# Kernel optimization log

Hardware: AMD Instinct MI355X
Metric: run time of the kernel (lower is better)

Reference implementation:

```python
import jax, jax.numpy as jnp
import numpy as np

# ---- config (mirrors AAModel init kwargs: ns=48, nv=10, sh_lmax=1) ----
N, E, NS, NV = 100000, 60000, 48, 10
SED, DED = 32, 32          # sigma / distance embedding dims
CUTOFF = 30.0              # GaussianSmearing(0, cutoff, DED)
SQ3 = float(np.sqrt(3.0))
W1_NUMEL = NS * NS + NS * NV                                   # 2784
# layer-2 fully-connected TP path weight offsets:
#   0e(x)0e->0e, 0e(x)1o->1o, 1o(x)0e->1o, 1o(x)1o->0e, 1o(x)1o->1e
O2 = [2304, 2784, 2884, 3364, 3464]


def _mlp2(x, W1, b1, W2, b2):
    return jax.nn.relu(x @ W1 + b1) @ W2 + b2


def _seg_mean(x, idx, n):
    s = jax.ops.segment_sum(x, idx, num_segments=n)
    cnt = jax.ops.segment_sum(jnp.ones(idx.shape, x.dtype), idx, num_segments=n)
    return s / jnp.maximum(cnt, 1.0).reshape((n,) + (1,) * (x.ndim - 1))


def _forward(pos, node_sigma_emb, node_s, edge_W1, edge_b1, edge_W2, edge_b2,
             fc1_W1, fc1_b1, fc1_W2, fc1_b2, fc2_W1, fc2_b1, fc2_W2, fc2_b2,
             edge_index):
    src, dst = edge_index[0], edge_index[1]
    vec = pos[dst] - pos[src]                          # [E,3]
    d = jnp.linalg.norm(vec, axis=-1)                  # [E]
    sh1 = SQ3 * vec / (d[:, None] + 1e-8)              # l=1 SH, component norm; sh0 == 1
    # Gaussian smearing of edge distances
    offsets = jnp.linspace(0.0, CUTOFF, DED)
    coeff = -0.5 / (offsets[1] - offsets[0]) ** 2
    demb = jnp.exp(coeff * (d[:, None] - offsets) ** 2)          # [E,DED]
    edge_emb = _mlp2(jnp.concatenate([node_sigma_emb[src], demb], -1),
                     edge_W1, edge_b1, edge_W2, edge_b2)         # [E,NS]

    # ---- conv layer 1:  ns x0e  (x)  1x0e+1x1o  ->  ns x0e + nv x1o ----
    xs = node_s[src]
    ea = jnp.concatenate([edge_emb, node_s[src], node_s[dst]], -1)   # [E,3*NS]
    w = _mlp2(ea, fc1_W1, fc1_b1, fc1_W2, fc1_b2)                    # [E,2784]
    w00 = w[:, :NS * NS].reshape(-1, NS, NS)
    w01 = w[:, NS * NS:].reshape(-1, NS, NV)
    inv = 1.0 / np.sqrt(NS)
    m_s = jnp.einsum('eio,ei->eo', w00, xs) * inv                    # [E,NS]
    m_v = jnp.einsum('eio,ei->eo', w01, xs)[:, :, None] * sh1[:, None, :] * inv  # [E,NV,3]
    node_s1 = node_s + _seg_mean(m_s, dst, N)                        # residual
    node_v1 = _seg_mean(m_v, dst, N)

    # ---- conv layer 2:  ns x0e + nv x1o  (x)  1x0e+1x1o  ->  ns x0e + nv x1o + nv x1e ----
    ea2 = jnp.concatenate([edge_emb, node_s1[src], node_s1[dst]], -1)
    w2 = _mlp2(ea2, fc2_W1, fc2_b1, fc2_W2, fc2_b2)                  # [E,3464]
    w00 = w2[:, :O2[0]].reshape(-1, NS, NS)
    w01 = w2[:, O2[0]:O2[1]].reshape(-1, NS, NV)
    w10 = w2[:, O2[1]:O2[2]].reshape(-1, NV, NV)
    w11s = w2[:, O2[2]:O2[3]].reshape(-1, NV, NS)
    w11p = w2[:, O2[3]:O2[4]].reshape(-1, NV, NV)
    xs, xv = node_s1[src], node_v1[src]
    nA = 1.0 / np.sqrt(2 * NS)
    nB = 1.0 / np.sqrt(2 * NV)
    m_s = (jnp.einsum('eio,ei->eo', w00, xs) * nA
           + jnp.einsum('eio,eid,ed->eo', w11s, xv, sh1) * (nB / SQ3))
    m_v = (jnp.einsum('eio,ei->eo', w01, xs)[:, :, None] * sh1[:, None, :] * nA
           + jnp.einsum('eio,eid->eod', w10, xv) * nB)
    m_p = jnp.einsum('eio,eid->eod', w11p, jnp.cross(xv, sh1[:, None, :])) * (1.0 / np.sqrt(2.0 * NV))
    node_s2 = node_s1 + _seg_mean(m_s, dst, N)
    node_v2 = node_v1 + _seg_mean(m_v, dst, N)
    node_p = _seg_mean(m_p, dst, N)
    # final node irreps ns x0e + nv x1o + nv x1e, flattened -> [N, 108]
    return jnp.concatenate([node_s2, node_v2.reshape(N, -1), node_p.reshape(N, -1)], -1)


def setup_inputs() -> dict:
    key = jax.random.key(0)
    k = jax.random.split(key, 10)
    f32 = jnp.float32
    def lin(kk, fi, fo):
        return jax.random.normal(kk, (fi, fo), f32) / np.sqrt(fi)
    return {
        'pos': 10.0 * jax.random.normal(k[0], (N, 3), f32),
        'node_sigma_emb': jax.random.normal(k[1], (N, SED), f32),
        'node_s': jax.random.normal(k[2], (N, NS), f32),
        'edge_W1': lin(k[3], SED + DED, NS), 'edge_b1': jnp.zeros((NS,), f32),
        'edge_W2': lin(k[4], NS, NS), 'edge_b2': jnp.zeros((NS,), f32),
        'fc1_W1': lin(k[5], 3 * NS, 3 * NS), 'fc1_b1': jnp.zeros((3 * NS,), f32),
        'fc1_W2': lin(k[6], 3 * NS, W1_NUMEL), 'fc1_b2': jnp.zeros((W1_NUMEL,), f32),
        'fc2_W1': lin(k[7], 3 * NS, 3 * NS), 'fc2_b1': jnp.zeros((3 * NS,), f32),
        'fc2_W2': lin(k[8], 3 * NS, O2[-1]), 'fc2_b2': jnp.zeros((O2[-1],), f32),
        'edge_index': jax.random.randint(k[9], (2, E), 0, N, jnp.int32),
    }


def reference(pos, node_sigma_emb, node_s, edge_W1, edge_b1, edge_W2, edge_b2,
              fc1_W1, fc1_b1, fc1_W2, fc1_b2, fc2_W1, fc2_b1, fc2_W2, fc2_b2,
              edge_index):
    return _forward(pos, node_sigma_emb, node_s, edge_W1, edge_b1, edge_W2, edge_b2,
                    fc1_W1, fc1_b1, fc1_W2, fc1_b2, fc2_W1, fc2_b1, fc2_W2, fc2_b2,
                    edge_index)
```

## Files before the change

kernel.cpp:

```cpp
#include <hip/hip_runtime.h>
#include <math.h>


constexpr float SQ3f = 1.7320508075688772f;
constexpr float INV1 = 0.14433756729740643f;
constexpr float NAc  = 0.10206207261596575f;
constexpr float NBc  = 0.22360679774997896f;
constexpr float C20  = 0.22360679774997896f;
constexpr float RATIO= 1.2649110640673518f;
constexpr float DSP  = 30.0f/31.0f;
constexpr float GCOEF= -0.5f/(DSP*DSP);

typedef __attribute__((ext_vector_type(8))) short bf16x8;
typedef __attribute__((ext_vector_type(4))) float f32x4;

__device__ __forceinline__ unsigned short f2bf(float x) {
    unsigned u = __builtin_bit_cast(unsigned, x);
    u += 0x7fffu + ((u >> 16) & 1u);
    return (unsigned short)(u >> 16);
}

__device__ __forceinline__ int colmap(int layer, int t, int lm) {
    if (layer == 0) return t*16 + lm;
    if (layer == 1) {
        if (t < 144) { const int og=t/48, i=t-og*48; return i*48 + og*16 + lm; }
        const int i = t-144; return (lm<10) ? 2304 + i*10 + lm : -1;
    }
    if (t < 144) { const int og=t/48, i=t-og*48; return i*48 + og*16 + lm; }
    if (t < 174) { const int s=t-144, og=s/10, i=s-og*10; return 2884 + i*48 + og*16 + lm; }
    if (t < 222) { const int i=t-174; return (lm<10) ? 2304 + i*10 + lm : -1; }
    if (t < 232) { const int i=t-222; return (lm<10) ? 2784 + i*10 + lm : -1; }
    { const int i=t-232; return (lm<10) ? 3364 + i*10 + lm : -1; }
}

__global__ __launch_bounds__(256)
void cvt_swz(const float* __restrict__ W, const float* __restrict__ bias,
             short* __restrict__ Wsw, int ncol, int ntile, int layer)
{
    const int gid = blockIdx.x*256 + threadIdx.x;
    const int g = gid >> 6, lane = gid & 63;
    if (g >= ntile*5) return;
    const int tile = g/5, ks = g - tile*5;
    const int c  = colmap(layer, tile, lane & 15);
    const int k0 = ks*32 + (lane >> 4)*8;
    union { uint4 u4; unsigned short h[8]; } pk;
    #pragma unroll
    for (int j=0;j<8;j++) {
        const int k = k0 + j;
        float v = 0.f;
        if (c >= 0) {
            if (k < 144)       v = W[(size_t)k*ncol + c];
            else if (k == 144) v = bias[c];
        }
        pk.h[j] = f2bf(v);
    }
    *(uint4*)&Wsw[((size_t)g*64 + lane)*8] = pk.u4;
}

__global__ __launch_bounds__(256)
void edge_kernel(const float* __restrict__ pos, const float* __restrict__ sigma,
                 const int* __restrict__ ei,
                 const float* __restrict__ W1, const float* __restrict__ b1,
                 const float* __restrict__ W2, const float* __restrict__ b2,
                 float* __restrict__ edge_emb, float* __restrict__ sh1buf,
                 int* __restrict__ deg, int E)
{
    __shared__ float inl[4][64];
    __shared__ float hidl[4][48];
    const int w    = threadIdx.x >> 6;
    const int lane = threadIdx.x & 63;
    const int e    = blockIdx.x*4 + w;
    const bool valid = (e < E);
    const int ec = valid ? e : 0;
    const int src = ei[ec], dst = ei[E+ec];
    const float vx = pos[dst*3+0]-pos[src*3+0];
    const float vy = pos[dst*3+1]-pos[src*3+1];
    const float vz = pos[dst*3+2]-pos[src*3+2];
    const float d  = sqrtf(vx*vx+vy*vy+vz*vz);
    const float si = SQ3f/(d+1e-8f);
    const float s0 = vx*si, s1 = vy*si, s2 = vz*si;
    if (lane < 32) {
        inl[w][lane] = sigma[src*32+lane];
    } else {
        const float off  = (float)(lane-32)*DSP;
        const float diff = d - off;
        inl[w][lane] = expf(GCOEF*diff*diff);
    }
    __syncthreads();
    if (lane < 48) {
        float a = b1[lane];
        #pragma unroll 8
        for (int j=0;j<64;j++) a = fmaf(inl[w][j], W1[j*48+lane], a);
        hidl[w][lane] = fmaxf(a, 0.f);
    }
    __syncthreads();
    if (valid) {
        if (lane < 48) {
            float a = b2[lane];
            #pragma unroll 8
            for (int j=0;j<48;j++) a = fmaf(hidl[w][j], W2[j*48+lane], a);
            edge_emb[e*48+lane] = a;
        }
        if (lane == 0) atomicAdd(&deg[dst], 1);
        if (lane < 3)  sh1buf[e*4+lane] = (lane==0)?s0:((lane==1)?s1:s2);
    }
}

__device__ __forceinline__ void load_bfrag(const short* __restrict__ Wsw,
                                           int tile, int lane, bf16x8 (&b)[5]) {
    #pragma unroll
    for (int ks=0; ks<5; ks++)
        b[ks] = *(const bf16x8*)&Wsw[((size_t)(tile*5+ks)*64 + lane)*8];
}

__device__ __forceinline__ void mfma5(const bf16x8 (&ag)[2][5], const bf16x8 (&b)[5],
                                      f32x4& a0, f32x4& a1) {
    a0 = (f32x4){0.f,0.f,0.f,0.f};
    a1 = (f32x4){0.f,0.f,0.f,0.f};
    #pragma unroll
    for (int ks=0; ks<5; ks++) {
        a0 = __builtin_amdgcn_mfma_f32_16x16x32_bf16(ag[0][ks], b[ks], a0, 0,0,0);
        a1 = __builtin_amdgcn_mfma_f32_16x16x32_bf16(ag[1][ks], b[ks], a1, 0,0,0);
    }
}

template<typename F>
__device__ __forceinline__ void region1(const short* __restrict__ Wsw, int base,
                                        int count, int lane,
                                        const bf16x8 (&ag)[2][5], F&& upd)
{
    bf16x8 bc[5], bn[5];
    load_bfrag(Wsw, base, lane, bc);
    for (int i=0; i<count; ++i) {
        if (i+1 < count) load_bfrag(Wsw, base+i+1, lane, bn);
        f32x4 a0, a1;
        mfma5(ag, bc, a0, a1);
        upd(i, a0, a1);
        #pragma unroll
        for (int ks=0; ks<5; ks++) bc[ks] = bn[ks];
    }
}

template<int LAYER>
__global__ __launch_bounds__(256)
void conv_kernel(const float* __restrict__ edge_emb, const float* __restrict__ sh1buf,
                 const int* __restrict__ ei,
                 const float* __restrict__ sin_, const float* __restrict__ vin,
                 const short* __restrict__ W1sw, const short* __restrict__ W2sw,
                 float* __restrict__ outS, float* __restrict__ outV, int E)
{
    __shared__ __align__(16) short eaB[32*192];
    __shared__ __align__(16) short hidB[32*192];
    __shared__ __align__(16) float xsT[48][36];
    __shared__ float sh1l[32][4];
    __shared__ int   srcl[32], dstl[32];
    __shared__ __align__(16) float xvT[LAYER==2 ? 30 : 1][36];
    __shared__ __align__(16) float uT [LAYER==2 ? 10 : 1][36];
    __shared__ __align__(16) float cvT[LAYER==2 ? 30 : 1][36];

    const int t  = threadIdx.x;
    const int eb = blockIdx.x * 32;

    if (t < 32) {
        const int ge = eb + t; const int gc = (ge < E) ? ge : (E-1);
        srcl[t] = ei[gc]; dstl[t] = ei[E+gc];
    }
    if (t < 128) {
        const int e = t >> 2, k = t & 3;
        const int ge = eb + e; const int gc = (ge<E)?ge:(E-1);
        sh1l[e][k] = sh1buf[gc*4 + k];
    }
    __syncthreads();

    for (int p = t; p < 32*24; p += 256) {
        const int m = p / 24, s = p - m*24;
        const int k0 = s*8;
        float vals[8] = {0.f,0.f,0.f,0.f,0.f,0.f,0.f,0.f};
        if (k0 < 48) {
            const int ge = eb + m; const int gc = (ge<E)?ge:(E-1);
            const float4 a = *(const float4*)&edge_emb[gc*48 + k0];
            const float4 b = *(const float4*)&edge_emb[gc*48 + k0 + 4];
            vals[0]=a.x; vals[1]=a.y; vals[2]=a.z; vals[3]=a.w;
            vals[4]=b.x; vals[5]=b.y; vals[6]=b.z; vals[7]=b.w;
        } else if (k0 < 96) {
            const float4 a = *(const float4*)&sin_[srcl[m]*48 + (k0-48)];
            const float4 b = *(const float4*)&sin_[srcl[m]*48 + (k0-48) + 4];
            vals[0]=a.x; vals[1]=a.y; vals[2]=a.z; vals[3]=a.w;
            vals[4]=b.x; vals[5]=b.y; vals[6]=b.z; vals[7]=b.w;
            #pragma unroll
            for (int j=0;j<8;j++) xsT[k0-48+j][m] = vals[j];
        } else if (k0 < 144) {
            const float4 a = *(const float4*)&sin_[dstl[m]*48 + (k0-96)];
            const float4 b = *(const float4*)&sin_[dstl[m]*48 + (k0-96) + 4];
            vals[0]=a.x; vals[1]=a.y; vals[2]=a.z; vals[3]=a.w;
            vals[4]=b.x; vals[5]=b.y; vals[6]=b.z; vals[7]=b.w;
        } else if (k0 == 144) {
            vals[0] = 1.f;
        }
        union { uint4 u4; unsigned short h[8]; } pk;
        #pragma unroll
        for (int j=0;j<8;j++) pk.h[j] = f2bf(vals[j]);
        *(uint4*)&eaB[m*192 + ((s ^ (m&7))*8)] = pk.u4;
    }
    if (t < 64) {
        const int m = t >> 1, s = 18 + (t & 1);
        union { uint4 u4; unsigned short h[8]; } pk;
        pk.u4.x = pk.u4.y = pk.u4.z = pk.u4.w = 0u;
        if (s == 18) pk.h[0] = f2bf(1.f);
        *(uint4*)&hidB[m*192 + ((s ^ (m&7))*8)] = pk.u4;
    }
    if (LAYER==2) {
        for (int p=t; p<320; p+=256) {
            const int i = p >> 5, e = p & 31;
            const float x0 = vin[srcl[e]*30 + i*3+0];
            const float x1 = vin[srcl[e]*30 + i*3+1];
            const float x2 = vin[srcl[e]*30 + i*3+2];
            const float h0=sh1l[e][0], h1=sh1l[e][1], h2=sh1l[e][2];
            xvT[i*3+0][e]=x0; xvT[i*3+1][e]=x1; xvT[i*3+2][e]=x2;
            uT[i][e] = x0*h0 + x1*h1 + x2*h2;
            cvT[i*3+0][e] = x1*h2 - x2*h1;
            cvT[i*3+1][e] = x2*h0 - x0*h2;
            cvT[i*3+2][e] = x0*h1 - x1*h0;
        }
    }
    __syncthreads();

    const int wv = t >> 6, lane = t & 63;
    const int lm = lane & 15, lk = lane >> 4, lk4 = lk*4;

    {
        bf16x8 af[2][5];
        #pragma unroll
        for (int mt=0; mt<2; mt++) {
            const int m = mt*16 + lm;
            #pragma unroll
            for (int ks=0; ks<5; ks++)
                af[mt][ks] = *(const bf16x8*)&eaB[m*192 + (((ks*4+lk) ^ (m&7))*8)];
        }
        for (int nt = wv; nt < 9; nt += 4) {
            bf16x8 bw[5];
            load_bfrag(W1sw, nt, lane, bw);
            f32x4 a0, a1;
            mfma5(af, bw, a0, a1);
            const int c = nt*16 + lm;
            #pragma unroll
            for (int r=0; r<4; r++) {
                const int m0 = lk4 + r, m1 = 16 + lk4 + r;
                hidB[m0*192 + (((c>>3) ^ (m0&7))*8) + (c&7)] = (short)f2bf(fmaxf(a0[r], 0.f));
                hidB[m1*192 + (((c>>3) ^ (m1&7))*8) + (c&7)] = (short)f2bf(fmaxf(a1[r], 0.f));
            }
        }
    }
    __syncthreads();

    bf16x8 ag[2][5];
    #pragma unroll
    for (int mt=0; mt<2; mt++) {
        const int m = mt*16 + lm;
        #pragma unroll
        for (int ks=0; ks<5; ks++)
            ag[mt][ks] = *(const bf16x8*)&hidB[m*192 + (((ks*4+lk) ^ (m&7))*8)];
    }

    if (wv < 3) {
        float ms[2][4] = {{0.f,0.f,0.f,0.f},{0.f,0.f,0.f,0.f}};
        region1(W2sw, wv*48, 48, lane, ag, [&](int i, f32x4 a0, f32x4 a1) {
            const f32x4 x0 = *(const f32x4*)&xsT[i][lk4];
            const f32x4 x1 = *(const f32x4*)&xsT[i][16+lk4];
            #pragma unroll
            for (int r=0;r<4;r++) {
                ms[0][r] = fmaf(a0[r], x0[r], ms[0][r]);
                ms[1][r] = fmaf(a1[r], x1[r], ms[1][r]);
            }
        });
        if (LAYER==2) {
            region1(W2sw, 144 + wv*10, 10, lane, ag, [&](int i, f32x4 a0, f32x4 a1) {
                const f32x4 u0 = *(const f32x4*)&uT[i][lk4];
                const f32x4 u1 = *(const f32x4*)&uT[i][16+lk4];
                #pragma unroll
                for (int r=0;r<4;r++) {
                    ms[0][r] = fmaf(a0[r]*RATIO, u0[r], ms[0][r]);
                    ms[1][r] = fmaf(a1[r]*RATIO, u1[r], ms[1][r]);
                }
            });
        }
        const float scale = (LAYER==1) ? INV1 : NAc;
        const int   strd  = (LAYER==1) ? 48 : 108;
        const int o = wv*16 + lm;
        #pragma unroll
        for (int r=0;r<4;r++) {
            const int e0 = lk4+r, e1 = 16+lk4+r;
            if (eb+e0 < E) unsafeAtomicAdd(&outS[(size_t)dstl[e0]*strd + o], ms[0][r]*scale);
            if (eb+e1 < E) unsafeAtomicAdd(&outS[(size_t)dstl[e1]*strd + o], ms[1][r]*scale);
        }
    } else {
        float vc[2][4] = {{0.f,0.f,0.f,0.f},{0.f,0.f,0.f,0.f}};
        region1(W2sw, (LAYER==1) ? 144 : 174, 48, lane, ag, [&](int i, f32x4 a0, f32x4 a1) {
            const f32x4 x0 = *(const f32x4*)&xsT[i][lk4];
            const f32x4 x1 = *(const f32x4*)&xsT[i][16+lk4];
            #pragma unroll
            for (int r=0;r<4;r++) {
                vc[0][r] = fmaf(a0[r], x0[r], vc[0][r]);
                vc[1][r] = fmaf(a1[r], x1[r], vc[1][r]);
            }
        });
        if (LAYER==1) {
            if (lm < 10) {
                #pragma unroll
                for (int r=0;r<4;r++) {
                    const int e0 = lk4+r, e1 = 16+lk4+r;
                    const float v0 = vc[0][r]*INV1, v1 = vc[1][r]*INV1;
                    #pragma unroll
                    for (int d=0; d<3; d++) {
                        if (eb+e0 < E) unsafeAtomicAdd(&outV[(size_t)dstl[e0]*30 + lm*3 + d], v0*sh1l[e0][d]);
                        if (eb+e1 < E) unsafeAtomicAdd(&outV[(size_t)dstl[e1]*30 + lm*3 + d], v1*sh1l[e1][d]);
                    }
                }
            }
        } else {
            {
                float m3[2][4][3] = {};
                region1(W2sw, 222, 10, lane, ag, [&](int i, f32x4 a0, f32x4 a1) {
                    #pragma unroll
                    for (int d=0; d<3; d++) {
                        const f32x4 x0 = *(const f32x4*)&xvT[i*3+d][lk4];
                        const f32x4 x1 = *(const f32x4*)&xvT[i*3+d][16+lk4];
                        #pragma unroll
                        for (int r=0;r<4;r++) {
                            m3[0][r][d] = fmaf(a0[r], x0[r], m3[0][r][d]);
                            m3[1][r][d] = fmaf(a1[r], x1[r], m3[1][r][d]);
                        }
                    }
                });
                if (lm < 10) {
                    #pragma unroll
                    for (int r=0;r<4;r++) {
                        const int e0 = lk4+r, e1 = 16+lk4+r;
                        const float v0 = vc[0][r]*NAc, v1 = vc[1][r]*NAc;
                        #pragma unroll
                        for (int d=0; d<3; d++) {
                            if (eb+e0 < E)
                                unsafeAtomicAdd(&outS[(size_t)dstl[e0]*108 + 48 + lm*3 + d],
                                                v0*sh1l[e0][d] + m3[0][r][d]*NBc);
                            if (eb+e1 < E)
                                unsafeAtomicAdd(&outS[(size_t)dstl[e1]*108 + 48 + lm*3 + d],
                                                v1*sh1l[e1][d] + m3[1][r][d]*NBc);
                        }
                    }
                }
            }
            {
                float m3[2][4][3] = {};
                region1(W2sw, 232, 10, lane, ag, [&](int i, f32x4 a0, f32x4 a1) {
                    #pragma unroll
                    for (int d=0; d<3; d++) {
                        const f32x4 x0 = *(const f32x4*)&cvT[i*3+d][lk4];
                        const f32x4 x1 = *(const f32x4*)&cvT[i*3+d][16+lk4];
                        #pragma unroll
                        for (int r=0;r<4;r++) {
                            m3[0][r][d] = fmaf(a0[r], x0[r], m3[0][r][d]);
                            m3[1][r][d] = fmaf(a1[r], x1[r], m3[1][r][d]);
                        }
                    }
                });
                if (lm < 10) {
                    #pragma unroll
                    for (int r=0;r<4;r++) {
                        const int e0 = lk4+r, e1 = 16+lk4+r;
                        #pragma unroll
                        for (int d=0; d<3; d++) {
                            if (eb+e0 < E)
                                unsafeAtomicAdd(&outS[(size_t)dstl[e0]*108 + 78 + lm*3 + d], m3[0][r][d]*C20);
                            if (eb+e1 < E)
                                unsafeAtomicAdd(&outS[(size_t)dstl[e1]*108 + 78 + lm*3 + d], m3[1][r][d]*C20);
                        }
                    }
                }
            }
        }
    }
}

__global__ __launch_bounds__(256)
void fin1_kernel(const float* __restrict__ node_s, const int* __restrict__ deg,
                 float* __restrict__ s1, float* __restrict__ v1, int Nn)
{
    const int p = blockIdx.x*256 + threadIdx.x;
    const int totS = Nn*48;
    if (p < totS) {
        const int n = p/48;
        const int dgi = deg[n];
        const float dg = (float)(dgi > 1 ? dgi : 1);
        s1[p] = node_s[p] + s1[p]/dg;
    } else {
        const int q = p - totS;
        if (q < Nn*30) {
            const int n = q/30;
            const int dgi = deg[n];
            const float dg = (float)(dgi > 1 ? dgi : 1);
            v1[q] = v1[q]/dg;
        }
    }
}

__global__ __launch_bounds__(256)
void fin2_kernel(const float* __restrict__ s1, const float* __restrict__ v1,
                 const int* __restrict__ deg, float* __restrict__ out, int Nn)
{
    const int p = blockIdx.x*256 + threadIdx.x;
    if (p >= Nn*108) return;
    const int n = p/108, c = p - n*108;
    const int dgi = deg[n];
    const float dg = (float)(dgi > 1 ? dgi : 1);
    const float acc = out[p]/dg;
    if (c < 48)      out[p] = s1[n*48+c] + acc;
    else if (c < 78) out[p] = v1[n*30 + (c-48)] + acc;
    else             out[p] = acc;
}

extern "C" void kernel_launch(void* const* d_in, const int* in_sizes, int n_in,
                              void* d_out, int out_size, void* d_ws, size_t ws_size,
                              hipStream_t stream)
{
    const float* pos    = (const float*)d_in[0];
    const float* sigma  = (const float*)d_in[1];
    const float* node_s = (const float*)d_in[2];
    const float* eW1  = (const float*)d_in[3];
    const float* eb1  = (const float*)d_in[4];
    const float* eW2  = (const float*)d_in[5];
    const float* eb2  = (const float*)d_in[6];
    const float* f1W1 = (const float*)d_in[7];
    const float* f1b1 = (const float*)d_in[8];
    const float* f1W2 = (const float*)d_in[9];
    const float* f1b2 = (const float*)d_in[10];
    const float* f2W1 = (const float*)d_in[11];
    const float* f2b1 = (const float*)d_in[12];
    const float* f2W2 = (const float*)d_in[13];
    const float* f2b2 = (const float*)d_in[14];
    const int*   ei   = (const int*)d_in[15];
    const int Nn = in_sizes[0]/3;
    const int E  = in_sizes[15]/2;
    float* out = (float*)d_out;

    char* ws = (char*)d_ws;
    float* edge_emb = (float*)ws;  ws += (size_t)E*48*sizeof(float);
    float* sh1buf   = (float*)ws;  ws += (size_t)E*4*sizeof(float);
    float* s1       = (float*)ws;  ws += (size_t)Nn*48*sizeof(float);
    float* v1       = (float*)ws;  ws += (size_t)Nn*30*sizeof(float);
    int*   deg      = (int*)ws;    ws += (size_t)Nn*sizeof(int);
    short* W1sw     = (short*)ws;  ws += (size_t)9*5*64*8*sizeof(short);
    short* W2sw     = (short*)ws;  ws += (size_t)242*5*64*8*sizeof(short);

    hipMemsetAsync(s1,  0, (size_t)Nn*48*sizeof(float), stream);
    hipMemsetAsync(v1,  0, (size_t)Nn*30*sizeof(float), stream);
    hipMemsetAsync(deg, 0, (size_t)Nn*sizeof(int),      stream);
    hipMemsetAsync(out, 0, (size_t)Nn*108*sizeof(float), stream);

    edge_kernel<<<(E+3)/4, 256, 0, stream>>>(pos, sigma, ei, eW1, eb1, eW2, eb2,
                                             edge_emb, sh1buf, deg, E);

    cvt_swz<<<(9*5*64+255)/256,   256, 0, stream>>>(f1W1, f1b1, W1sw, 144, 9, 0);
    cvt_swz<<<(192*5*64+255)/256, 256, 0, stream>>>(f1W2, f1b2, W2sw, 2784, 192, 1);

    conv_kernel<1><<<(E+31)/32, 256, 0, stream>>>(edge_emb, sh1buf, ei, node_s, nullptr,
                                                  W1sw, W2sw, s1, v1, E);
    fin1_kernel<<<((size_t)Nn*78 + 255)/256, 256, 0, stream>>>(node_s, deg, s1, v1, Nn);

    cvt_swz<<<(9*5*64+255)/256,   256, 0, stream>>>(f2W1, f2b1, W1sw, 144, 9, 0);
    cvt_swz<<<(242*5*64+255)/256, 256, 0, stream>>>(f2W2, f2b2, W2sw, 3464, 242, 2);

    conv_kernel<2><<<(E+31)/32, 256, 0, stream>>>(edge_emb, sh1buf, ei, s1, v1,
                                                  W1sw, W2sw, out, nullptr, E);
    fin2_kernel<<<((size_t)Nn*108 + 255)/256, 256, 0, stream>>>(s1, v1, deg, out, Nn);
}
```

Baseline: 484.1 us.

## Process 64 edges per block to reuse weight fragments across four M-tiles

The conv kernel now handles 64 edges per block instead of 32. Each loaded B weight fragment feeds four MFMA row tiles instead of two, which halves the global/L2 traffic for the large per-edge weight matrices. The eaB and hidB buffers are merged into one shared pool, with an extra barrier so the hidden activations can overwrite the inputs, which keeps LDS use in check. In exchange, each wave holds twice as many A fragments and accumulators, raising register pressure and possibly lowering occupancy, and there are half as many blocks.

```diff
diff --git a/kernel.cpp b/kernel.cpp
--- a/kernel.cpp
+++ b/kernel.cpp
@@ -113,29 +113,24 @@
         b[ks] = *(const bf16x8*)&Wsw[((size_t)(tile*5+ks)*64 + lane)*8];
 }
 
-__device__ __forceinline__ void mfma5(const bf16x8 (&ag)[2][5], const bf16x8 (&b)[5],
-                                      f32x4& a0, f32x4& a1) {
-    a0 = (f32x4){0.f,0.f,0.f,0.f};
-    a1 = (f32x4){0.f,0.f,0.f,0.f};
-    #pragma unroll
-    for (int ks=0; ks<5; ks++) {
-        a0 = __builtin_amdgcn_mfma_f32_16x16x32_bf16(ag[0][ks], b[ks], a0, 0,0,0);
-        a1 = __builtin_amdgcn_mfma_f32_16x16x32_bf16(ag[1][ks], b[ks], a1, 0,0,0);
-    }
-}
-
 template<typename F>
 __device__ __forceinline__ void region1(const short* __restrict__ Wsw, int base,
                                         int count, int lane,
-                                        const bf16x8 (&ag)[2][5], F&& upd)
+                                        const bf16x8 (&ag)[4][5], F&& upd)
 {
     bf16x8 bc[5], bn[5];
     load_bfrag(Wsw, base, lane, bc);
     for (int i=0; i<count; ++i) {
         if (i+1 < count) load_bfrag(Wsw, base+i+1, lane, bn);
-        f32x4 a0, a1;
-        mfma5(ag, bc, a0, a1);
-        upd(i, a0, a1);
+        f32x4 a[4];
+        #pragma unroll
+        for (int mt=0; mt<4; mt++) a[mt] = (f32x4){0.f,0.f,0.f,0.f};
+        #pragma unroll
+        for (int ks=0; ks<5; ks++)
+            #pragma unroll
+            for (int mt=0; mt<4; mt++)
+                a[mt] = __builtin_amdgcn_mfma_f32_16x16x32_bf16(ag[mt][ks], bc[ks], a[mt], 0,0,0);
+        upd(i, a);
         #pragma unroll
         for (int ks=0; ks<5; ks++) bc[ks] = bn[ks];
     }
@@ -149,30 +144,29 @@
                  const short* __restrict__ W1sw, const short* __restrict__ W2sw,
                  float* __restrict__ outS, float* __restrict__ outV, int E)
 {
-    __shared__ __align__(16) short eaB[32*192];
-    __shared__ __align__(16) short hidB[32*192];
-    __shared__ __align__(16) float xsT[48][36];
-    __shared__ float sh1l[32][4];
-    __shared__ int   srcl[32], dstl[32];
-    __shared__ __align__(16) float xvT[LAYER==2 ? 30 : 1][36];
-    __shared__ __align__(16) float uT [LAYER==2 ? 10 : 1][36];
-    __shared__ __align__(16) float cvT[LAYER==2 ? 30 : 1][36];
+    __shared__ __align__(16) short pool[64*192];
+    __shared__ __align__(16) float xsT[48][68];
+    __shared__ float sh1l[64][4];
+    __shared__ int   srcl[64], dstl[64];
+    __shared__ __align__(16) float xvT[LAYER==2 ? 30 : 1][68];
+    __shared__ __align__(16) float uT [LAYER==2 ? 10 : 1][68];
+    __shared__ __align__(16) float cvT[LAYER==2 ? 30 : 1][68];
 
     const int t  = threadIdx.x;
-    const int eb = blockIdx.x * 32;
-
-    if (t < 32) {
+    const int eb = blockIdx.x * 64;
+
+    if (t < 64) {
         const int ge = eb + t; const int gc = (ge < E) ? ge : (E-1);
         srcl[t] = ei[gc]; dstl[t] = ei[E+gc];
     }
-    if (t < 128) {
+    {
         const int e = t >> 2, k = t & 3;
         const int ge = eb + e; const int gc = (ge<E)?ge:(E-1);
         sh1l[e][k] = sh1buf[gc*4 + k];
     }
     __syncthreads();
 
-    for (int p = t; p < 32*24; p += 256) {
+    for (int p = t; p < 64*24; p += 256) {
         const int m = p / 24, s = p - m*24;
         const int k0 = s*8;
         float vals[8] = {0.f,0.f,0.f,0.f,0.f,0.f,0.f,0.f};
@@ -200,18 +194,11 @@
         union { uint4 u4; unsigned short h[8]; } pk;
         #pragma unroll
         for (int j=0;j<8;j++) pk.h[j] = f2bf(vals[j]);
-        *(uint4*)&eaB[m*192 + ((s ^ (m&7))*8)] = pk.u4;
-    }
-    if (t < 64) {
-        const int m = t >> 1, s = 18 + (t & 1);
-        union { uint4 u4; unsigned short h[8]; } pk;
-        pk.u4.x = pk.u4.y = pk.u4.z = pk.u4.w = 0u;
-        if (s == 18) pk.h[0] = f2bf(1.f);
-        *(uint4*)&hidB[m*192 + ((s ^ (m&7))*8)] = pk.u4;
+        *(uint4*)&pool[m*192 + ((s ^ (m&7))*8)] = pk.u4;
     }
     if (LAYER==2) {
-        for (int p=t; p<320; p+=256) {
-            const int i = p >> 5, e = p & 31;
+        for (int p=t; p<640; p+=256) {
+            const int i = p >> 6, e = p & 63;
             const float x0 = vin[srcl[e]*30 + i*3+0];
             const float x1 = vin[srcl[e]*30 + i*3+1];
             const float x2 = vin[srcl[e]*30 + i*3+2];
@@ -229,58 +216,81 @@
     const int lm = lane & 15, lk = lane >> 4, lk4 = lk*4;
 
     {
-        bf16x8 af[2][5];
-        #pragma unroll
-        for (int mt=0; mt<2; mt++) {
+        bf16x8 af[4][5];
+        #pragma unroll
+        for (int mt=0; mt<4; mt++) {
             const int m = mt*16 + lm;
             #pragma unroll
             for (int ks=0; ks<5; ks++)
-                af[mt][ks] = *(const bf16x8*)&eaB[m*192 + (((ks*4+lk) ^ (m&7))*8)];
-        }
-        for (int nt = wv; nt < 9; nt += 4) {
-            bf16x8 bw[5];
-            load_bfrag(W1sw, nt, lane, bw);
-            f32x4 a0, a1;
-            mfma5(af, bw, a0, a1);
-            const int c = nt*16 + lm;
-            #pragma unroll
-            for (int r=0; r<4; r++) {
-                const int m0 = lk4 + r, m1 = 16 + lk4 + r;
-                hidB[m0*192 + (((c>>3) ^ (m0&7))*8) + (c&7)] = (short)f2bf(fmaxf(a0[r], 0.f));
-                hidB[m1*192 + (((c>>3) ^ (m1&7))*8) + (c&7)] = (short)f2bf(fmaxf(a1[r], 0.f));
-            }
+                af[mt][ks] = *(const bf16x8*)&pool[m*192 + (((ks*4+lk) ^ (m&7))*8)];
+        }
+        f32x4 acc[3][4];
+        #pragma unroll
+        for (int j=0; j<3; j++) {
+            const int nt = wv + j*4;
+            if (nt < 9) {
+                bf16x8 bw[5];
+                load_bfrag(W1sw, nt, lane, bw);
+                #pragma unroll
+                for (int mt=0; mt<4; mt++) acc[j][mt] = (f32x4){0.f,0.f,0.f,0.f};
+                #pragma unroll
+                for (int ks=0; ks<5; ks++)
+                    #pragma unroll
+                    for (int mt=0; mt<4; mt++)
+                        acc[j][mt] = __builtin_amdgcn_mfma_f32_16x16x32_bf16(af[mt][ks], bw[ks], acc[j][mt], 0,0,0);
+            }
+        }
+        __syncthreads();
+        #pragma unroll
+        for (int j=0; j<3; j++) {
+            const int nt = wv + j*4;
+            if (nt < 9) {
+                const int c = nt*16 + lm;
+                #pragma unroll
+                for (int mt=0; mt<4; mt++)
+                    #pragma unroll
+                    for (int r=0; r<4; r++) {
+                        const int m = mt*16 + lk4 + r;
+                        pool[m*192 + (((c>>3) ^ (m&7))*8) + (c&7)] = (short)f2bf(fmaxf(acc[j][mt][r], 0.f));
+                    }
+            }
+        }
+        if (t < 128) {
+            const int m = t >> 1, s = 18 + (t & 1);
+            union { uint4 u4; unsigned short h[8]; } pk;
+            pk.u4.x = pk.u4.y = pk.u4.z = pk.u4.w = 0u;
+            if (s == 18) pk.h[0] = f2bf(1.f);
+            *(uint4*)&pool[m*192 + ((s ^ (m&7))*8)] = pk.u4;
         }
     }
     __syncthreads();
 
-    bf16x8 ag[2][5];
+    bf16x8 ag[4][5];
     #pragma unroll
-    for (int mt=0; mt<2; mt++) {
+    for (int mt=0; mt<4; mt++) {
         const int m = mt*16 + lm;
         #pragma unroll
         for (int ks=0; ks<5; ks++)
-            ag[mt][ks] = *(const bf16x8*)&hidB[m*192 + (((ks*4+lk) ^ (m&7))*8)];
+            ag[mt][ks] = *(const bf16x8*)&pool[m*192 + (((ks*4+lk) ^ (m&7))*8)];
     }
 
     if (wv < 3) {
-        float ms[2][4] = {{0.f,0.f,0.f,0.f},{0.f,0.f,0.f,0.f}};
-        region1(W2sw, wv*48, 48, lane, ag, [&](int i, f32x4 a0, f32x4 a1) {
-            const f32x4 x0 = *(const f32x4*)&xsT[i][lk4];
-            const f32x4 x1 = *(const f32x4*)&xsT[i][16+lk4];
-            #pragma unroll
-            for (int r=0;r<4;r++) {
-                ms[0][r] = fmaf(a0[r], x0[r], ms[0][r]);
-                ms[1][r] = fmaf(a1[r], x1[r], ms[1][r]);
+        float ms[4][4] = {};
+        region1(W2sw, wv*48, 48, lane, ag, [&](int i, const f32x4 (&a)[4]) {
+            #pragma unroll
+            for (int mt=0; mt<4; mt++) {
+                const f32x4 x = *(const f32x4*)&xsT[i][mt*16 + lk4];
+                #pragma unroll
+                for (int r=0;r<4;r++) ms[mt][r] = fmaf(a[mt][r], x[r], ms[mt][r]);
             }
         });
         if (LAYER==2) {
-            region1(W2sw, 144 + wv*10, 10, lane, ag, [&](int i, f32x4 a0, f32x4 a1) {
-                const f32x4 u0 = *(const f32x4*)&uT[i][lk4];
-                const f32x4 u1 = *(const f32x4*)&uT[i][16+lk4];
-                #pragma unroll
-                for (int r=0;r<4;r++) {
-                    ms[0][r] = fmaf(a0[r]*RATIO, u0[r], ms[0][r]);
-                    ms[1][r] = fmaf(a1[r]*RATIO, u1[r], ms[1][r]);
+            region1(W2sw, 144 + wv*10, 10, lane, ag, [&](int i, const f32x4 (&a)[4]) {
+                #pragma unroll
+                for (int mt=0; mt<4; mt++) {
+                    const f32x4 u = *(const f32x4*)&uT[i][mt*16 + lk4];
+                    #pragma unroll
+                    for (int r=0;r<4;r++) ms[mt][r] = fmaf(a[mt][r]*RATIO, u[r], ms[mt][r]);
                 }
             });
         }
@@ -288,93 +298,91 @@
         const int   strd  = (LAYER==1) ? 48 : 108;
         const int o = wv*16 + lm;
         #pragma unroll
-        for (int r=0;r<4;r++) {
-            const int e0 = lk4+r, e1 = 16+lk4+r;
-            if (eb+e0 < E) unsafeAtomicAdd(&outS[(size_t)dstl[e0]*strd + o], ms[0][r]*scale);
-            if (eb+e1 < E) unsafeAtomicAdd(&outS[(size_t)dstl[e1]*strd + o], ms[1][r]*scale);
-        }
+        for (int mt=0; mt<4; mt++)
+            #pragma unroll
+            for (int r=0;r<4;r++) {
+                const int e = mt*16 + lk4 + r;
+                if (eb+e < E) unsafeAtomicAdd(&outS[(size_t)dstl[e]*strd + o], ms[mt][r]*scale);
+            }
     } else {
-        float vc[2][4] = {{0.f,0.f,0.f,0.f},{0.f,0.f,0.f,0.f}};
-        region1(W2sw, (LAYER==1) ? 144 : 174, 48, lane, ag, [&](int i, f32x4 a0, f32x4 a1) {
-            const f32x4 x0 = *(const f32x4*)&xsT[i][lk4];
-            const f32x4 x1 = *(const f32x4*)&xsT[i][16+lk4];
-            #pragma unroll
-            for (int r=0;r<4;r++) {
-                vc[0][r] = fmaf(a0[r], x0[r], vc[0][r]);
-                vc[1][r] = fmaf(a1[r], x1[r], vc[1][r]);
+        float vc[4][4] = {};
+        region1(W2sw, (LAYER==1) ? 144 : 174, 48, lane, ag, [&](int i, const f32x4 (&a)[4]) {
+            #pragma unroll
+            for (int mt=0; mt<4; mt++) {
+                const f32x4 x = *(const f32x4*)&xsT[i][mt*16 + lk4];
+                #pragma unroll
+                for (int r=0;r<4;r++) vc[mt][r] = fmaf(a[mt][r], x[r], vc[mt][r]);
             }
         });
         if (LAYER==1) {
             if (lm < 10) {
                 #pragma unroll
-                for (int r=0;r<4;r++) {
-                    const int e0 = lk4+r, e1 = 16+lk4+r;
-                    const float v0 = vc[0][r]*INV1, v1 = vc[1][r]*INV1;
-                    #pragma unroll
-                    for (int d=0; d<3; d++) {
-                        if (eb+e0 < E) unsafeAtomicAdd(&outV[(size_t)dstl[e0]*30 + lm*3 + d], v0*sh1l[e0][d]);
-                        if (eb+e1 < E) unsafeAtomicAdd(&outV[(size_t)dstl[e1]*30 + lm*3 + d], v1*sh1l[e1][d]);
+                for (int mt=0; mt<4; mt++)
+                    #pragma unroll
+                    for (int r=0;r<4;r++) {
+                        const int e = mt*16 + lk4 + r;
+                        if (eb+e < E) {
+                            const float v = vc[mt][r]*INV1;
+                            #pragma unroll
+                            for (int d=0; d<3; d++)
+                                unsafeAtomicAdd(&outV[(size_t)dstl[e]*30 + lm*3 + d], v*sh1l[e][d]);
+                        }
                     }
-                }
             }
         } else {
             {
-                float m3[2][4][3] = {};
-                region1(W2sw, 222, 10, lane, ag, [&](int i, f32x4 a0, f32x4 a1) {
-                    #pragma unroll
-                    for (int d=0; d<3; d++) {
-                        const f32x4 x0 = *(const f32x4*)&xvT[i*3+d][lk4];
-                        const f32x4 x1 = *(const f32x4*)&xvT[i*3+d][16+lk4];
+                float m3[4][4][3] = {};
+                region1(W2sw, 222, 10, lane, ag, [&](int i, const f32x4 (&a)[4]) {
+                    #pragma unroll
+                    for (int d=0; d<3; d++)
+                        #pragma unroll
+                        for (int mt=0; mt<4; mt++) {
+                            const f32x4 x = *(const f32x4*)&xvT[i*3+d][mt*16 + lk4];
+                            #pragma unroll
+                            for (int r=0;r<4;r++) m3[mt][r][d] = fmaf(a[mt][r], x[r], m3[mt][r][d]);
+                        }
+                });
+                if (lm < 10) {
+                    #pragma unroll
+                    for (int mt=0; mt<4; mt++)
                         #pragma unroll
                         for (int r=0;r<4;r++) {
-                            m3[0][r][d] = fmaf(a0[r], x0[r], m3[0][r][d]);
-                            m3[1][r][d] = fmaf(a1[r], x1[r], m3[1][r][d]);
+                            const int e = mt*16 + lk4 + r;
+                            if (eb+e < E) {
+                                const float v = vc[mt][r]*NAc;
+                                #pragma unroll
+                                for (int d=0; d<3; d++)
+                                    unsafeAtomicAdd(&outS[(size_t)dstl[e]*108 + 48 + lm*3 + d],
+                                                    v*sh1l[e][d] + m3[mt][r][d]*NBc);
+                            }
                         }
-                    }
+                }
+            }
+            {
+                float m3[4][4][3] = {};
+                region1(W2sw, 232, 10, lane, ag, [&](int i, const f32x4 (&a)[4]) {
+                    #pragma unroll
+                    for (int d=0; d<3; d++)
+                        #pragma unroll
+                        for (int mt=0; mt<4; mt++) {
+                            const f32x4 x = *(const f32x4*)&cvT[i*3+d][mt*16 + lk4];
+                            #pragma unroll
+                            for (int r=0;r<4;r++) m3[mt][r][d] = fmaf(a[mt][r], x[r], m3[mt][r][d]);
+                        }
                 });
                 if (lm < 10) {
                     #pragma unroll
-                    for (int r=0;r<4;r++) {
-                        const int e0 = lk4+r, e1 = 16+lk4+r;
-                        const float v0 = vc[0][r]*NAc, v1 = vc[1][r]*NAc;
-                        #pragma unroll
-                        for (int d=0; d<3; d++) {
-                            if (eb+e0 < E)
-                                unsafeAtomicAdd(&outS[(size_t)dstl[e0]*108 + 48 + lm*3 + d],
-                                                v0*sh1l[e0][d] + m3[0][r][d]*NBc);
-                            if (eb+e1 < E)
-                                unsafeAtomicAdd(&outS[(size_t)dstl[e1]*108 + 48 + lm*3 + d],
-                                                v1*sh1l[e1][d] + m3[1][r][d]*NBc);
-                        }
-                    }
-                }
-            }
-            {
-                float m3[2][4][3] = {};
-                region1(W2sw, 232, 10, lane, ag, [&](int i, f32x4 a0, f32x4 a1) {
-                    #pragma unroll
-                    for (int d=0; d<3; d++) {
-                        const f32x4 x0 = *(const f32x4*)&cvT[i*3+d][lk4];
-                        const f32x4 x1 = *(const f32x4*)&cvT[i*3+d][16+lk4];
+                    for (int mt=0; mt<4; mt++)
                         #pragma unroll
                         for (int r=0;r<4;r++) {
-                            m3[0][r][d] = fmaf(a0[r], x0[r], m3[0][r][d]);
-                            m3[1][r][d] = fmaf(a1[r], x1[r], m3[1][r][d]);
+                            const int e = mt*16 + lk4 + r;
+                            if (eb+e < E) {
+                                #pragma unroll
+                                for (int d=0; d<3; d++)
+                                    unsafeAtomicAdd(&outS[(size_t)dstl[e]*108 + 78 + lm*3 + d],
+                                                    m3[mt][r][d]*C20);
+                            }
                         }
-                    }
-                });
-                if (lm < 10) {
-                    #pragma unroll
-                    for (int r=0;r<4;r++) {
-                        const int e0 = lk4+r, e1 = 16+lk4+r;
-                        #pragma unroll
-                        for (int d=0; d<3; d++) {
-                            if (eb+e0 < E)
-                                unsafeAtomicAdd(&outS[(size_t)dstl[e0]*108 + 78 + lm*3 + d], m3[0][r][d]*C20);
-                            if (eb+e1 < E)
-                                unsafeAtomicAdd(&outS[(size_t)dstl[e1]*108 + 78 + lm*3 + d], m3[1][r][d]*C20);
-                        }
-                    }
                 }
             }
         }
@@ -462,14 +470,14 @@
     cvt_swz<<<(9*5*64+255)/256,   256, 0, stream>>>(f1W1, f1b1, W1sw, 144, 9, 0);
     cvt_swz<<<(192*5*64+255)/256, 256, 0, stream>>>(f1W2, f1b2, W2sw, 2784, 192, 1);
 
-    conv_kernel<1><<<(E+31)/32, 256, 0, stream>>>(edge_emb, sh1buf, ei, node_s, nullptr,
+    conv_kernel<1><<<(E+63)/64, 256, 0, stream>>>(edge_emb, sh1buf, ei, node_s, nullptr,
                                                   W1sw, W2sw, s1, v1, E);
     fin1_kernel<<<((size_t)Nn*78 + 255)/256, 256, 0, stream>>>(node_s, deg, s1, v1, Nn);
 
     cvt_swz<<<(9*5*64+255)/256,   256, 0, stream>>>(f2W1, f2b1, W1sw, 144, 9, 0);
     cvt_swz<<<(242*5*64+255)/256, 256, 0, stream>>>(f2W2, f2b2, W2sw, 3464, 242, 2);
 
-    conv_kernel<2><<<(E+31)/32, 256, 0, stream>>>(edge_emb, sh1buf, ei, s1, v1,
+    conv_kernel<2><<<(E+63)/64, 256, 0, stream>>>(edge_emb, sh1buf, ei, s1, v1,
                                                   W1sw, W2sw, out, nullptr, E);
     fin2_kernel<<<((size_t)Nn*108 + 255)/256, 256, 0, stream>>>(s1, v1, deg, out, Nn);
 }
```

After: 519.7 us. 1.07x slower.
